# Optimization experiments

Measured on AMD Instinct MI355X. Metric: run time of the kernel, lower is better.

The kernel has to match this reference:

```python
import jax, jax.numpy as jnp
import numpy as np

H = 32  # GRU hidden size


def _conv1d(x, w, b, stride, pad):
    # x: (B, Cin, L), w: (Cout, Cin, K)
    y = jax.lax.conv_general_dilated(
        x, w, window_strides=(stride,), padding=[(pad, pad)],
        dimension_numbers=('NCH', 'OIH', 'NCH'))
    return y + b[None, :, None]


def setup_inputs() -> dict:
    key = jax.random.key(0)
    ks = jax.random.split(key, 16)
    B = 16384
    inp = {
        'past_samples': jax.random.normal(ks[0], (B, 2000), jnp.float32),
        'velocity': jax.random.uniform(ks[1], (B,), jnp.float32),
        'log_pitch': jax.random.normal(ks[2], (B,), jnp.float32),
        'time': jax.random.uniform(ks[3], (B,), jnp.float32),
        'hidden_state': jax.random.normal(ks[4], (B, H), jnp.float32),
        # conv stack params
        'w1': jax.random.normal(ks[5], (4, 1, 31), jnp.float32) * 0.1,
        'b1': jnp.zeros((4,), jnp.float32),
        'w2': jax.random.normal(ks[6], (8, 4, 15), jnp.float32) * 0.1,
        'b2': jnp.zeros((8,), jnp.float32),
        'w3': jax.random.normal(ks[7], (16, 8, 7), jnp.float32) * 0.1,
        'b3': jnp.zeros((16,), jnp.float32),
        # GRU params (torch layout: rows = [r; z; n])
        'w_ih': jax.random.normal(ks[8], (3 * H, 19), jnp.float32) * 0.1,
        'w_hh': jax.random.normal(ks[9], (3 * H, H), jnp.float32) * 0.1,
        'b_ih': jnp.zeros((3 * H,), jnp.float32),
        'b_hh': jnp.zeros((3 * H,), jnp.float32),
        # projection
        'w_proj': jax.random.normal(ks[10], (2, H), jnp.float32) * 0.1,
        'b_proj': jnp.zeros((2,), jnp.float32),
    }
    return inp


def reference(past_samples, velocity, log_pitch, time, hidden_state,
              w1, b1, w2, b2, w3, b3, w_ih, w_hh, b_ih, b_hh, w_proj, b_proj):
    x = past_samples[:, None, :]                       # (B,1,2000)
    x = jax.nn.relu(_conv1d(x, w1, b1, 4, 15))         # (B,4,500)
    x = jax.nn.relu(_conv1d(x, w2, b2, 4, 7))          # (B,8,125)
    x = jax.nn.relu(_conv1d(x, w3, b3, 4, 3))          # (B,16,32)
    ctx = jnp.mean(x, axis=2)                          # adaptive avg pool -> (B,16)

    rnn_in = jnp.concatenate(
        [ctx, velocity[:, None], log_pitch[:, None], time[:, None]], axis=1)  # (B,19)

    # single GRU step (torch GRUCell math)
    gi = rnn_in @ w_ih.T + b_ih                        # (B,3H)
    gh = hidden_state @ w_hh.T + b_hh                  # (B,3H)
    r = jax.nn.sigmoid(gi[:, :H] + gh[:, :H])
    z = jax.nn.sigmoid(gi[:, H:2 * H] + gh[:, H:2 * H])
    n = jnp.tanh(gi[:, 2 * H:] + r * gh[:, 2 * H:])
    new_hidden = (1.0 - z) * n + z * hidden_state      # (B,H)

    out = new_hidden @ w_proj.T + b_proj               # (B,2)
    mu, log_sigma = out[:, :1], out[:, 1:]
    sigma = jnp.exp(log_sigma)
    return (mu, sigma, new_hidden)
```

## Files before the change

kernel.cpp:

```cpp
#include <hip/hip_runtime.h>
#include <hip/hip_fp16.h>
#include <math.h>


typedef _Float16 h2 __attribute__((ext_vector_type(2)));
typedef _Float16 h4 __attribute__((ext_vector_type(4)));

__device__ __forceinline__ float fdot2(h2 a, h2 b, float c)
{
#if defined(__has_builtin)
#if __has_builtin(__builtin_amdgcn_fdot2)
    return __builtin_amdgcn_fdot2(a, b, c, false);
#else
    return c + (float)a.x * (float)b.x + (float)a.y * (float)b.y;
#endif
#else
    return c + (float)a.x * (float)b.x + (float)a.y * (float)b.y;
#endif
}

__global__ void pack_weights(const float* __restrict__ w1,
                             const float* __restrict__ w2,
                             const float* __restrict__ w3,
                             h2* __restrict__ ws)
{
    for (int idx = threadIdx.x; idx < 832; idx += 256) {
        float f0, f1;
        if (idx < 64) {
            int c = idx >> 4, jp = idx & 15;
            int j0 = 2 * jp, j1 = j0 + 1;
            f0 = (j0 == 0) ? 0.0f : w1[c * 31 + j0 - 1];
            f1 = w1[c * 31 + j1 - 1];
        } else if (idx < 320) {
            int r = idx - 64, cc = r >> 3, jp = r & 7;
            int j0 = 2 * jp, j1 = j0 + 1;
            f0 = w2[cc * 15 + j0];
            f1 = (j1 < 15) ? w2[cc * 15 + j1] : 0.0f;
        } else {
            int r = idx - 320, cc = r >> 2, jp = r & 3;
            int j0 = 2 * jp, j1 = j0 + 1;
            f0 = (j0 < 7) ? w3[cc * 7 + j0] : 0.0f;
            f1 = (j1 < 7) ? w3[cc * 7 + j1] : 0.0f;
        }
        ws[idx] = (h2){(_Float16)f0, (_Float16)f1};
    }
}

__device__ __forceinline__ void conv1_pos(const _Float16* __restrict__ xh,
                                          _Float16* __restrict__ y1h,
                                          const h2* __restrict__ w1p,
                                          const float* __restrict__ b1,
                                          int p, int h0)
{
    const h4* src = (const h4*)(xh + h0);
    h2 xp[16];
#pragma unroll
    for (int j = 0; j < 8; ++j) {
        h4 v = src[j];
        xp[2 * j]     = (h2){v.x, v.y};
        xp[2 * j + 1] = (h2){v.z, v.w};
    }
    float a0 = b1[0], a1 = b1[1], a2 = b1[2], a3 = b1[3];
#pragma unroll
    for (int j = 0; j < 16; ++j) {
        a0 = fdot2(xp[j], w1p[j],      a0);
        a1 = fdot2(xp[j], w1p[16 + j], a1);
        a2 = fdot2(xp[j], w1p[32 + j], a2);
        a3 = fdot2(xp[j], w1p[48 + j], a3);
    }
    y1h[7 + p]        = (_Float16)fmaxf(a0, 0.0f);
    y1h[512 + 7 + p]  = (_Float16)fmaxf(a1, 0.0f);
    y1h[1024 + 7 + p] = (_Float16)fmaxf(a2, 0.0f);
    y1h[1536 + 7 + p] = (_Float16)fmaxf(a3, 0.0f);
}

__global__ void __launch_bounds__(64, 3)
wavernn_fused(const float* __restrict__ past,
              const float* __restrict__ velocity,
              const float* __restrict__ log_pitch,
              const float* __restrict__ time_in,
              const float* __restrict__ hidden,
              const float* __restrict__ b1,
              const float* __restrict__ b2,
              const float* __restrict__ b3,
              const float* __restrict__ w_ih, const float* __restrict__ w_hh,
              const float* __restrict__ b_ih, const float* __restrict__ b_hh,
              const float* __restrict__ w_proj, const float* __restrict__ b_proj,
              const h2* __restrict__ wsp,
              float* __restrict__ out, int B)
{
    __shared__ __align__(16) _Float16 X[1056];
    __shared__ __align__(16) _Float16 y1h[2048];
    __shared__ float rnn[20];
    __shared__ float hs[32];

    _Float16* const xbuf = X;
    _Float16* const y2h  = X;
    float* const gis     = (float*)X;
    float* const ghs     = (float*)X + 96;

    const h2* const w1p = wsp;
    const h2* const w2p = wsp + 64;
    const h2* const w3p = wsp + 320;

    const int t = threadIdx.x;
    const int b = blockIdx.x;

    const float4* row4 = (const float4*)(past + (size_t)b * 2000);

    if (t < 16) { xbuf[t] = (_Float16)0.0f; xbuf[1032 + t] = (_Float16)0.0f; }
    if (t < 48) { int c = t / 12, k = t % 12;
                  y1h[c * 512 + (k < 7 ? k : 500 + k)] = (_Float16)0.0f; }
    if (t < 32) hs[t] = hidden[(size_t)b * 32 + t];
    if (t == 0) rnn[16] = velocity[b];
    if (t == 1) rnn[17] = log_pitch[b];
    if (t == 2) rnn[18] = time_in[b];

#pragma unroll
    for (int j = 0; j < 4; ++j) {
        int i = t + 64 * j;
        if (i < 254) {
            float4 q = row4[i];
            h4 hv = {(_Float16)q.x, (_Float16)q.y, (_Float16)q.z, (_Float16)q.w};
            *(h4*)(xbuf + 16 + 4 * i) = hv;
        }
    }
    __syncthreads();

#pragma unroll
    for (int j = 0; j < 4; ++j) {
        int p = t + 64 * j;
        if (p < 250) conv1_pos(xbuf, y1h, w1p, b1, p, 4 * p);
    }
    __syncthreads();

#pragma unroll
    for (int j = 0; j < 4; ++j) {
        int i = t + 64 * j;
        if (i < 254) {
            float4 q = row4[246 + i];
            h4 hv = {(_Float16)q.x, (_Float16)q.y, (_Float16)q.z, (_Float16)q.w};
            *(h4*)(xbuf + 16 + 4 * i) = hv;
        }
    }
    __syncthreads();

#pragma unroll
    for (int j = 0; j < 4; ++j) {
        int p = 250 + t + 64 * j;
        if (p < 500) conv1_pos(xbuf, y1h, w1p, b1, p, 4 * p - 984);
    }
    __syncthreads();

    if (t < 56) { int c = t / 7, k = t % 7;
                  y2h[c * 132 + (k < 3 ? k : 125 + k)] = (_Float16)0.0f; }
#pragma unroll
    for (int jj = 0; jj < 2; ++jj) {
        int p = t + 64 * jj;
        if (p < 125) {
            float acc[8];
#pragma unroll
            for (int c = 0; c < 8; ++c) acc[c] = b2[c];
#pragma unroll
            for (int ci = 0; ci < 4; ++ci) {
                const h4* src = (const h4*)(y1h + 512 * ci + 4 * p);
                h2 xp[8];
#pragma unroll
                for (int j = 0; j < 4; ++j) {
                    h4 v = src[j];
                    xp[2 * j]     = (h2){v.x, v.y};
                    xp[2 * j + 1] = (h2){v.z, v.w};
                }
#pragma unroll
                for (int jp = 0; jp < 8; ++jp) {
#pragma unroll
                    for (int c = 0; c < 8; ++c)
                        acc[c] = fdot2(xp[jp], w2p[(c * 4 + ci) * 8 + jp], acc[c]);
                }
            }
#pragma unroll
            for (int c = 0; c < 8; ++c)
                y2h[c * 132 + 3 + p] = (_Float16)fmaxf(acc[c], 0.0f);
        }
    }
    __syncthreads();

    if (t < 32) {
        float acc[16];
#pragma unroll
        for (int c = 0; c < 16; ++c) acc[c] = 0.0f;
#pragma unroll
        for (int ci = 0; ci < 8; ++ci) {
            const h4* src = (const h4*)(y2h + 132 * ci + 4 * t);
            h4 v0 = src[0], v1 = src[1];
            h2 xp[4] = {(h2){v0.x, v0.y}, (h2){v0.z, v0.w},
                        (h2){v1.x, v1.y}, (h2){v1.z, v1.w}};
#pragma unroll
            for (int jp = 0; jp < 4; ++jp) {
#pragma unroll
                for (int c = 0; c < 16; ++c)
                    acc[c] = fdot2(xp[jp], w3p[(c * 8 + ci) * 4 + jp], acc[c]);
            }
        }
#pragma unroll
        for (int c = 0; c < 16; ++c) {
            float v = fmaxf(acc[c] + b3[c], 0.0f);
            v += __shfl_xor(v, 16); v += __shfl_xor(v, 8);
            v += __shfl_xor(v, 4);  v += __shfl_xor(v, 2);
            v += __shfl_xor(v, 1);
            if (t == 0) rnn[c] = v * (1.0f / 32.0f);
        }
    }
    __syncthreads();

    {
        float rv[19];
#pragma unroll
        for (int j = 0; j < 19; ++j) rv[j] = rnn[j];

        float a = b_ih[t];
        const float* wr = w_ih + t * 19;
#pragma unroll
        for (int j = 0; j < 19; ++j) a += rv[j] * wr[j];
        gis[t] = a;
        if (t < 32) {
            float a2 = b_ih[64 + t];
            const float* wr2 = w_ih + (64 + t) * 19;
#pragma unroll
            for (int j = 0; j < 19; ++j) a2 += rv[j] * wr2[j];
            gis[64 + t] = a2;
        }

        float hv[32];
#pragma unroll
        for (int j = 0; j < 32; ++j) hv[j] = hs[j];

        float g = b_hh[t];
        const float4* wh = (const float4*)(w_hh + t * 32);
#pragma unroll
        for (int j = 0; j < 8; ++j) {
            float4 q = wh[j];
            g += hv[4 * j] * q.x + hv[4 * j + 1] * q.y +
                 hv[4 * j + 2] * q.z + hv[4 * j + 3] * q.w;
        }
        ghs[t] = g;
        if (t < 32) {
            float g2 = b_hh[64 + t];
            const float4* wh2 = (const float4*)(w_hh + (64 + t) * 32);
#pragma unroll
            for (int j = 0; j < 8; ++j) {
                float4 q = wh2[j];
                g2 += hv[4 * j] * q.x + hv[4 * j + 1] * q.y +
                      hv[4 * j + 2] * q.z + hv[4 * j + 3] * q.w;
            }
            ghs[64 + t] = g2;
        }
    }
    __syncthreads();

    if (t < 32) {
        const int j = t;
        float r = 1.0f / (1.0f + expf(-(gis[j] + ghs[j])));
        float z = 1.0f / (1.0f + expf(-(gis[32 + j] + ghs[32 + j])));
        float n = tanhf(gis[64 + j] + r * ghs[64 + j]);
        float nh = (1.0f - z) * n + z * hs[j];
        out[(size_t)2 * B + (size_t)b * 32 + j] = nh;

        float p0 = nh * w_proj[j];
        float p1 = nh * w_proj[32 + j];
        p0 += __shfl_xor(p0, 16); p1 += __shfl_xor(p1, 16);
        p0 += __shfl_xor(p0, 8);  p1 += __shfl_xor(p1, 8);
        p0 += __shfl_xor(p0, 4);  p1 += __shfl_xor(p1, 4);
        p0 += __shfl_xor(p0, 2);  p1 += __shfl_xor(p1, 2);
        p0 += __shfl_xor(p0, 1);  p1 += __shfl_xor(p1, 1);
        if (j == 0) {
            out[b] = p0 + b_proj[0];
            out[B + b] = expf(p1 + b_proj[1]);
        }
    }
}

extern "C" void kernel_launch(void* const* d_in, const int* in_sizes, int n_in,
                              void* d_out, int out_size, void* d_ws, size_t ws_size,
                              hipStream_t stream)
{
    const float* past      = (const float*)d_in[0];
    const float* velocity  = (const float*)d_in[1];
    const float* log_pitch = (const float*)d_in[2];
    const float* time_in   = (const float*)d_in[3];
    const float* hidden    = (const float*)d_in[4];
    const float* w1  = (const float*)d_in[5];
    const float* b1  = (const float*)d_in[6];
    const float* w2  = (const float*)d_in[7];
    const float* b2  = (const float*)d_in[8];
    const float* w3  = (const float*)d_in[9];
    const float* b3  = (const float*)d_in[10];
    const float* wih = (const float*)d_in[11];
    const float* whh = (const float*)d_in[12];
    const float* bih = (const float*)d_in[13];
    const float* bhh = (const float*)d_in[14];
    const float* wpr = (const float*)d_in[15];
    const float* bpr = (const float*)d_in[16];

    const int B = in_sizes[0] / 2000;
    h2* wsp = (h2*)d_ws;

    pack_weights<<<dim3(1), dim3(256), 0, stream>>>(w1, w2, w3, wsp);

    wavernn_fused<<<dim3(B), dim3(64), 0, stream>>>(
        past, velocity, log_pitch, time_in, hidden,
        b1, b2, b3, wih, whh, bih, bhh, wpr, bpr,
        (const h2*)wsp, (float*)d_out, B);
}
```

Baseline: 273.2 us.

## Process two rows per block with one wave each and wave-local syncs

Each 128-thread block now handles two batch rows, one per 64-lane wavefront, with per-wave shared buffers. Block barriers are replaced by an s_waitcnt lgkmcnt(0) wave-local wait, relying on all threads of a wave executing in lockstep. W_ih is repacked to a padded 20-wide layout so it can be read with float4 loads. The goal is to cut barrier cost and launch overhead per row and raise occupancy. The cost is reliance on wavefront lockstep for LDS ordering, which holds on CDNA with wave64 but is fragile.

```diff
diff --git a/kernel.cpp b/kernel.cpp
--- a/kernel.cpp
+++ b/kernel.cpp
@@ -19,10 +19,17 @@
 #endif
 }
 
+__device__ __forceinline__ void wave_sync()
+{
+    asm volatile("s_waitcnt lgkmcnt(0)" ::: "memory");
+}
+
 __global__ void pack_weights(const float* __restrict__ w1,
                              const float* __restrict__ w2,
                              const float* __restrict__ w3,
-                             h2* __restrict__ ws)
+                             const float* __restrict__ w_ih,
+                             h2* __restrict__ ws,
+                             float* __restrict__ wihp)
 {
     for (int idx = threadIdx.x; idx < 832; idx += 256) {
         float f0, f1;
@@ -44,6 +51,10 @@
         }
         ws[idx] = (h2){(_Float16)f0, (_Float16)f1};
     }
+    for (int idx = threadIdx.x; idx < 96 * 20; idx += 256) {
+        int r = idx / 20, c = idx % 20;
+        wihp[idx] = (c < 19) ? w_ih[r * 19 + c] : 0.0f;
+    }
 }
 
 __device__ __forceinline__ void conv1_pos(const _Float16* __restrict__ xh,
@@ -74,7 +85,7 @@
     y1h[1536 + 7 + p] = (_Float16)fmaxf(a3, 0.0f);
 }
 
-__global__ void __launch_bounds__(64, 3)
+__global__ void __launch_bounds__(128, 6)
 wavernn_fused(const float* __restrict__ past,
               const float* __restrict__ velocity,
               const float* __restrict__ log_pitch,
@@ -83,28 +94,34 @@
               const float* __restrict__ b1,
               const float* __restrict__ b2,
               const float* __restrict__ b3,
-              const float* __restrict__ w_ih, const float* __restrict__ w_hh,
+              const float* __restrict__ wihp,
+              const float* __restrict__ w_hh,
               const float* __restrict__ b_ih, const float* __restrict__ b_hh,
               const float* __restrict__ w_proj, const float* __restrict__ b_proj,
               const h2* __restrict__ wsp,
               float* __restrict__ out, int B)
 {
-    __shared__ __align__(16) _Float16 X[1056];
-    __shared__ __align__(16) _Float16 y1h[2048];
-    __shared__ float rnn[20];
-    __shared__ float hs[32];
-
-    _Float16* const xbuf = X;
-    _Float16* const y2h  = X;
-    float* const gis     = (float*)X;
-    float* const ghs     = (float*)X + 96;
+    __shared__ __align__(16) _Float16 Xs[2][1056];
+    __shared__ __align__(16) _Float16 y1s[2][2048];
+    __shared__ float rnns[2][20];
+    __shared__ float hss[2][32];
+
+    const int w = threadIdx.x >> 6;
+    const int t = threadIdx.x & 63;
+    const int b = blockIdx.x * 2 + w;
+    if (b >= B) return;
+
+    _Float16* const xbuf = &Xs[w][0];
+    _Float16* const y2h  = &Xs[w][0];
+    float* const gis     = (float*)&Xs[w][0];
+    float* const ghs     = (float*)&Xs[w][0] + 96;
+    _Float16* const y1h  = &y1s[w][0];
+    float* const rnn     = &rnns[w][0];
+    float* const hs      = &hss[w][0];
 
     const h2* const w1p = wsp;
     const h2* const w2p = wsp + 64;
     const h2* const w3p = wsp + 320;
-
-    const int t = threadIdx.x;
-    const int b = blockIdx.x;
 
     const float4* row4 = (const float4*)(past + (size_t)b * 2000);
 
@@ -115,6 +132,7 @@
     if (t == 0) rnn[16] = velocity[b];
     if (t == 1) rnn[17] = log_pitch[b];
     if (t == 2) rnn[18] = time_in[b];
+    if (t == 3) rnn[19] = 0.0f;
 
 #pragma unroll
     for (int j = 0; j < 4; ++j) {
@@ -125,14 +143,14 @@
             *(h4*)(xbuf + 16 + 4 * i) = hv;
         }
     }
-    __syncthreads();
+    wave_sync();
 
 #pragma unroll
     for (int j = 0; j < 4; ++j) {
         int p = t + 64 * j;
         if (p < 250) conv1_pos(xbuf, y1h, w1p, b1, p, 4 * p);
     }
-    __syncthreads();
+    wave_sync();
 
 #pragma unroll
     for (int j = 0; j < 4; ++j) {
@@ -143,14 +161,14 @@
             *(h4*)(xbuf + 16 + 4 * i) = hv;
         }
     }
-    __syncthreads();
+    wave_sync();
 
 #pragma unroll
     for (int j = 0; j < 4; ++j) {
         int p = 250 + t + 64 * j;
         if (p < 500) conv1_pos(xbuf, y1h, w1p, b1, p, 4 * p - 984);
     }
-    __syncthreads();
+    wave_sync();
 
     if (t < 56) { int c = t / 7, k = t % 7;
                   y2h[c * 132 + (k < 3 ? k : 125 + k)] = (_Float16)0.0f; }
@@ -183,7 +201,7 @@
                 y2h[c * 132 + 3 + p] = (_Float16)fmaxf(acc[c], 0.0f);
         }
     }
-    __syncthreads();
+    wave_sync();
 
     if (t < 32) {
         float acc[16];
@@ -211,23 +229,31 @@
             if (t == 0) rnn[c] = v * (1.0f / 32.0f);
         }
     }
-    __syncthreads();
+    wave_sync();
 
     {
-        float rv[19];
-#pragma unroll
-        for (int j = 0; j < 19; ++j) rv[j] = rnn[j];
+        float rv[20];
+#pragma unroll
+        for (int j = 0; j < 20; ++j) rv[j] = rnn[j];
 
         float a = b_ih[t];
-        const float* wr = w_ih + t * 19;
-#pragma unroll
-        for (int j = 0; j < 19; ++j) a += rv[j] * wr[j];
+        const float4* wr = (const float4*)(wihp + t * 20);
+#pragma unroll
+        for (int j = 0; j < 5; ++j) {
+            float4 q = wr[j];
+            a += rv[4 * j] * q.x + rv[4 * j + 1] * q.y +
+                 rv[4 * j + 2] * q.z + rv[4 * j + 3] * q.w;
+        }
         gis[t] = a;
         if (t < 32) {
             float a2 = b_ih[64 + t];
-            const float* wr2 = w_ih + (64 + t) * 19;
-#pragma unroll
-            for (int j = 0; j < 19; ++j) a2 += rv[j] * wr2[j];
+            const float4* wr2 = (const float4*)(wihp + (64 + t) * 20);
+#pragma unroll
+            for (int j = 0; j < 5; ++j) {
+                float4 q = wr2[j];
+                a2 += rv[4 * j] * q.x + rv[4 * j + 1] * q.y +
+                      rv[4 * j + 2] * q.z + rv[4 * j + 3] * q.w;
+            }
             gis[64 + t] = a2;
         }
 
@@ -256,7 +282,7 @@
             ghs[64 + t] = g2;
         }
     }
-    __syncthreads();
+    wave_sync();
 
     if (t < 32) {
         const int j = t;
@@ -304,11 +330,12 @@
 
     const int B = in_sizes[0] / 2000;
     h2* wsp = (h2*)d_ws;
-
-    pack_weights<<<dim3(1), dim3(256), 0, stream>>>(w1, w2, w3, wsp);
-
-    wavernn_fused<<<dim3(B), dim3(64), 0, stream>>>(
+    float* wihp = (float*)((char*)d_ws + 4096);
+
+    pack_weights<<<dim3(1), dim3(256), 0, stream>>>(w1, w2, w3, wih, wsp, wihp);
+
+    wavernn_fused<<<dim3((B + 1) / 2), dim3(128), 0, stream>>>(
         past, velocity, log_pitch, time_in, hidden,
-        b1, b2, b3, wih, whh, bih, bhh, wpr, bpr,
+        b1, b2, b3, wihp, whh, bih, bhh, wpr, bpr,
         (const h2*)wsp, (float*)d_out, B);
 }
```

Measured after the change: 283.3 us. 3.7% more time.

## Compute conv2 and conv3 with MFMA 16x16x32 f16 instead of fdot2 loops

Applied to the files above, without the earlier changes.

Repacks the conv2 and conv3 weights into MFMA A-fragment layout and computes both convolutions with __builtin_amdgcn_mfma_f32_16x16x32_f16. The whole 64-lane wave now does this work, where before conv2 ran as per-thread fdot2 loops with two positions per thread and conv3 used only 32 threads. The W_ih matrix is also padded to 20 columns so it can be read with float4 loads. The cost is zero-padding waste in the MFMA tiles and a larger weight-packing pass. Conv1 still dominates and is unchanged.

```diff
diff --git a/kernel.cpp b/kernel.cpp
--- a/kernel.cpp
+++ b/kernel.cpp
@@ -5,6 +5,8 @@
 
 typedef _Float16 h2 __attribute__((ext_vector_type(2)));
 typedef _Float16 h4 __attribute__((ext_vector_type(4)));
+typedef _Float16 h8 __attribute__((ext_vector_type(8)));
+typedef float f4 __attribute__((ext_vector_type(4)));
 
 __device__ __forceinline__ float fdot2(h2 a, h2 b, float c)
 {
@@ -19,30 +21,45 @@
 #endif
 }
 
+__device__ __forceinline__ h8 ld_b8(const _Float16* p)
+{
+    h4 lo = *(const h4*)p;
+    h4 hi = *(const h4*)(p + 4);
+    return (h8){lo.x, lo.y, lo.z, lo.w, hi.x, hi.y, hi.z, hi.w};
+}
+
 __global__ void pack_weights(const float* __restrict__ w1,
                              const float* __restrict__ w2,
                              const float* __restrict__ w3,
-                             h2* __restrict__ ws)
-{
-    for (int idx = threadIdx.x; idx < 832; idx += 256) {
-        float f0, f1;
-        if (idx < 64) {
-            int c = idx >> 4, jp = idx & 15;
-            int j0 = 2 * jp, j1 = j0 + 1;
-            f0 = (j0 == 0) ? 0.0f : w1[c * 31 + j0 - 1];
-            f1 = w1[c * 31 + j1 - 1];
-        } else if (idx < 320) {
-            int r = idx - 64, cc = r >> 3, jp = r & 7;
-            int j0 = 2 * jp, j1 = j0 + 1;
-            f0 = w2[cc * 15 + j0];
-            f1 = (j1 < 15) ? w2[cc * 15 + j1] : 0.0f;
-        } else {
-            int r = idx - 320, cc = r >> 2, jp = r & 3;
-            int j0 = 2 * jp, j1 = j0 + 1;
-            f0 = (j0 < 7) ? w3[cc * 7 + j0] : 0.0f;
-            f1 = (j1 < 7) ? w3[cc * 7 + j1] : 0.0f;
-        }
-        ws[idx] = (h2){(_Float16)f0, (_Float16)f1};
+                             const float* __restrict__ w_ih,
+                             _Float16* __restrict__ hws,
+                             float* __restrict__ wihp)
+{
+    for (int idx = threadIdx.x; idx < 64; idx += 256) {
+        int c = idx >> 4, jp = idx & 15;
+        int j0 = 2 * jp, j1 = j0 + 1;
+        float f0 = (j0 == 0) ? 0.0f : w1[c * 31 + j0 - 1];
+        float f1 = w1[c * 31 + j1 - 1];
+        hws[2 * idx]     = (_Float16)f0;
+        hws[2 * idx + 1] = (_Float16)f1;
+    }
+    for (int i = threadIdx.x; i < 1024; i += 256) {
+        int kk = i >> 9, l = (i >> 3) & 63, j = i & 7;
+        int c = l & 15, k = kk * 32 + ((l >> 4) << 3) + j;
+        int ci = k >> 4, tap = k & 15;
+        float v = (c < 8 && tap < 15) ? w2[(c * 4 + ci) * 15 + tap] : 0.0f;
+        hws[1024 + i] = (_Float16)v;
+    }
+    for (int i = threadIdx.x; i < 1024; i += 256) {
+        int kk = i >> 9, l = (i >> 3) & 63, j = i & 7;
+        int c = l & 15, k = kk * 32 + ((l >> 4) << 3) + j;
+        int ci = k >> 3, tap = k & 7;
+        float v = (tap < 7) ? w3[(c * 8 + ci) * 7 + tap] : 0.0f;
+        hws[2048 + i] = (_Float16)v;
+    }
+    for (int idx = threadIdx.x; idx < 96 * 20; idx += 256) {
+        int r = idx / 20, c = idx % 20;
+        wihp[idx] = (c < 19) ? w_ih[r * 19 + c] : 0.0f;
     }
 }
 
@@ -83,10 +100,11 @@
               const float* __restrict__ b1,
               const float* __restrict__ b2,
               const float* __restrict__ b3,
-              const float* __restrict__ w_ih, const float* __restrict__ w_hh,
+              const float* __restrict__ wihp,
+              const float* __restrict__ w_hh,
               const float* __restrict__ b_ih, const float* __restrict__ b_hh,
               const float* __restrict__ w_proj, const float* __restrict__ b_proj,
-              const h2* __restrict__ wsp,
+              const _Float16* __restrict__ hws,
               float* __restrict__ out, int B)
 {
     __shared__ __align__(16) _Float16 X[1056];
@@ -99,9 +117,9 @@
     float* const gis     = (float*)X;
     float* const ghs     = (float*)X + 96;
 
-    const h2* const w1p = wsp;
-    const h2* const w2p = wsp + 64;
-    const h2* const w3p = wsp + 320;
+    const h2* const w1p = (const h2*)hws;
+    const h8* const wf2 = (const h8*)(hws + 1024);
+    const h8* const wf3 = (const h8*)(hws + 2048);
 
     const int t = threadIdx.x;
     const int b = blockIdx.x;
@@ -115,6 +133,7 @@
     if (t == 0) rnn[16] = velocity[b];
     if (t == 1) rnn[17] = log_pitch[b];
     if (t == 2) rnn[18] = time_in[b];
+    if (t == 3) rnn[19] = 0.0f;
 
 #pragma unroll
     for (int j = 0; j < 4; ++j) {
@@ -154,80 +173,81 @@
 
     if (t < 56) { int c = t / 7, k = t % 7;
                   y2h[c * 132 + (k < 3 ? k : 125 + k)] = (_Float16)0.0f; }
-#pragma unroll
-    for (int jj = 0; jj < 2; ++jj) {
-        int p = t + 64 * jj;
-        if (p < 125) {
-            float acc[8];
-#pragma unroll
-            for (int c = 0; c < 8; ++c) acc[c] = b2[c];
-#pragma unroll
-            for (int ci = 0; ci < 4; ++ci) {
-                const h4* src = (const h4*)(y1h + 512 * ci + 4 * p);
-                h2 xp[8];
-#pragma unroll
-                for (int j = 0; j < 4; ++j) {
-                    h4 v = src[j];
-                    xp[2 * j]     = (h2){v.x, v.y};
-                    xp[2 * j + 1] = (h2){v.z, v.w};
-                }
-#pragma unroll
-                for (int jp = 0; jp < 8; ++jp) {
-#pragma unroll
-                    for (int c = 0; c < 8; ++c)
-                        acc[c] = fdot2(xp[jp], w2p[(c * 4 + ci) * 8 + jp], acc[c]);
-                }
+    {
+        const int o = t >> 4, q = t & 15;
+        const int ci0 = o >> 1, tp0 = (o & 1) * 8;
+        float b2v[4];
+#pragma unroll
+        for (int r = 0; r < 4; ++r) b2v[r] = b2[(o * 4 + r) & 7];
+        const h8 a0 = wf2[t];
+        const h8 a1 = wf2[64 + t];
+#pragma unroll
+        for (int T = 0; T < 8; ++T) {
+            const int p = T * 16 + q;
+            h8 x0 = ld_b8(y1h + 512 * ci0 + 4 * p + tp0);
+            h8 x1 = ld_b8(y1h + 512 * (ci0 + 2) + 4 * p + tp0);
+            f4 acc = {0.0f, 0.0f, 0.0f, 0.0f};
+            acc = __builtin_amdgcn_mfma_f32_16x16x32_f16(a0, x0, acc, 0, 0, 0);
+            acc = __builtin_amdgcn_mfma_f32_16x16x32_f16(a1, x1, acc, 0, 0, 0);
+            if (t < 32 && p < 125) {
+#pragma unroll
+                for (int r = 0; r < 4; ++r)
+                    y2h[(o * 4 + r) * 132 + 3 + p] =
+                        (_Float16)fmaxf(acc[r] + b2v[r], 0.0f);
             }
-#pragma unroll
-            for (int c = 0; c < 8; ++c)
-                y2h[c * 132 + 3 + p] = (_Float16)fmaxf(acc[c], 0.0f);
-        }
-    }
-    __syncthreads();
-
-    if (t < 32) {
-        float acc[16];
-#pragma unroll
-        for (int c = 0; c < 16; ++c) acc[c] = 0.0f;
-#pragma unroll
-        for (int ci = 0; ci < 8; ++ci) {
-            const h4* src = (const h4*)(y2h + 132 * ci + 4 * t);
-            h4 v0 = src[0], v1 = src[1];
-            h2 xp[4] = {(h2){v0.x, v0.y}, (h2){v0.z, v0.w},
-                        (h2){v1.x, v1.y}, (h2){v1.z, v1.w}};
-#pragma unroll
-            for (int jp = 0; jp < 4; ++jp) {
-#pragma unroll
-                for (int c = 0; c < 16; ++c)
-                    acc[c] = fdot2(xp[jp], w3p[(c * 8 + ci) * 4 + jp], acc[c]);
-            }
-        }
-#pragma unroll
-        for (int c = 0; c < 16; ++c) {
-            float v = fmaxf(acc[c] + b3[c], 0.0f);
-            v += __shfl_xor(v, 16); v += __shfl_xor(v, 8);
-            v += __shfl_xor(v, 4);  v += __shfl_xor(v, 2);
-            v += __shfl_xor(v, 1);
-            if (t == 0) rnn[c] = v * (1.0f / 32.0f);
         }
     }
     __syncthreads();
 
     {
-        float rv[19];
-#pragma unroll
-        for (int j = 0; j < 19; ++j) rv[j] = rnn[j];
+        const int o = t >> 4, q = t & 15;
+        float b3v[4];
+#pragma unroll
+        for (int r = 0; r < 4; ++r) b3v[r] = b3[o * 4 + r];
+        const h8 a0 = wf3[t];
+        const h8 a1 = wf3[64 + t];
+        h8 x00 = ld_b8(y2h + 132 * o + 4 * q);
+        h8 x01 = ld_b8(y2h + 132 * (4 + o) + 4 * q);
+        h8 x10 = ld_b8(y2h + 132 * o + 4 * (16 + q));
+        h8 x11 = ld_b8(y2h + 132 * (4 + o) + 4 * (16 + q));
+        const f4 z = {0.0f, 0.0f, 0.0f, 0.0f};
+        f4 d0 = __builtin_amdgcn_mfma_f32_16x16x32_f16(a0, x00, z, 0, 0, 0);
+        d0 = __builtin_amdgcn_mfma_f32_16x16x32_f16(a1, x01, d0, 0, 0, 0);
+        f4 d1 = __builtin_amdgcn_mfma_f32_16x16x32_f16(a0, x10, z, 0, 0, 0);
+        d1 = __builtin_amdgcn_mfma_f32_16x16x32_f16(a1, x11, d1, 0, 0, 0);
+#pragma unroll
+        for (int r = 0; r < 4; ++r) {
+            float v = fmaxf(d0[r] + b3v[r], 0.0f) + fmaxf(d1[r] + b3v[r], 0.0f);
+            v += __shfl_xor(v, 1); v += __shfl_xor(v, 2);
+            v += __shfl_xor(v, 4); v += __shfl_xor(v, 8);
+            if (q == 0) rnn[o * 4 + r] = v * (1.0f / 32.0f);
+        }
+    }
+    __syncthreads();
+
+    {
+        float rv[20];
+#pragma unroll
+        for (int j = 0; j < 20; ++j) rv[j] = rnn[j];
 
         float a = b_ih[t];
-        const float* wr = w_ih + t * 19;
-#pragma unroll
-        for (int j = 0; j < 19; ++j) a += rv[j] * wr[j];
+        const float4* wr = (const float4*)(wihp + t * 20);
+#pragma unroll
+        for (int j = 0; j < 5; ++j) {
+            float4 q = wr[j];
+            a += rv[4 * j] * q.x + rv[4 * j + 1] * q.y +
+                 rv[4 * j + 2] * q.z + rv[4 * j + 3] * q.w;
+        }
         gis[t] = a;
         if (t < 32) {
             float a2 = b_ih[64 + t];
-            const float* wr2 = w_ih + (64 + t) * 19;
-#pragma unroll
-            for (int j = 0; j < 19; ++j) a2 += rv[j] * wr2[j];
+            const float4* wr2 = (const float4*)(wihp + (64 + t) * 20);
+#pragma unroll
+            for (int j = 0; j < 5; ++j) {
+                float4 q = wr2[j];
+                a2 += rv[4 * j] * q.x + rv[4 * j + 1] * q.y +
+                      rv[4 * j + 2] * q.z + rv[4 * j + 3] * q.w;
+            }
             gis[64 + t] = a2;
         }
 
@@ -303,12 +323,13 @@
     const float* bpr = (const float*)d_in[16];
 
     const int B = in_sizes[0] / 2000;
-    h2* wsp = (h2*)d_ws;
-
-    pack_weights<<<dim3(1), dim3(256), 0, stream>>>(w1, w2, w3, wsp);
+    _Float16* hws = (_Float16*)d_ws;
+    float* wihp = (float*)((char*)d_ws + 8192);
+
+    pack_weights<<<dim3(1), dim3(256), 0, stream>>>(w1, w2, w3, wih, hws, wihp);
 
     wavernn_fused<<<dim3(B), dim3(64), 0, stream>>>(
         past, velocity, log_pitch, time_in, hidden,
-        b1, b2, b3, wih, whh, bih, bhh, wpr, bpr,
-        (const h2*)wsp, (float*)d_out, B);
-}
+        b1, b2, b3, wihp, whh, bih, bhh, wpr, bpr,
+        (const _Float16*)hws, (float*)d_out, B);
+}
```

New measurement: 257.1 us. -5.9%, faster.
